# Kernel optimization log

Measured on AMD Instinct MI355X. Metric: run time of the kernel, lower is better.

## Reference

```python
import jax, jax.numpy as jnp
import numpy as np

GROUP_SIZE = 128  # quantization group size along K


def setup_inputs() -> dict:
    key = jax.random.key(0)
    k1, k2, k3, k4 = jax.random.split(key, 4)
    B, S, K = 2, 2048, 4096
    N = 11008
    num_groups = K // GROUP_SIZE
    x = jax.random.normal(k1, (B, S, K), dtype=jnp.float32)
    # int8 quantized weights, stored as int32 for portability (values in [-128, 127])
    qw = jax.random.randint(k2, (N, K), -128, 128, dtype=jnp.int32)
    # per-group scales (positive, small, like amax/127)
    sw = jax.random.uniform(k3, (N, num_groups), dtype=jnp.float32, minval=1e-4, maxval=0.02)
    bias = jax.random.normal(k4, (N,), dtype=jnp.float32)
    return {"x": x, "qw": qw, "sw": sw, "bias": bias}


def reference(x, qw, sw, bias):
    # x: [..., K], qw: [N, K] int8-valued, sw: [N, K//GROUP_SIZE], bias: [N]
    N, K = qw.shape
    num_groups = K // GROUP_SIZE
    # per-group dequantize: w[n, g, j] = qw[n, g, j] * sw[n, g]
    w_dequant = (qw.reshape(N, num_groups, GROUP_SIZE).astype(jnp.float32)
                 * sw[:, :, None]).reshape(N, K)
    x_dtype = x.dtype
    y = jnp.einsum('...k,nk->...n', x.astype(jnp.float32), w_dequant).astype(x_dtype)
    y = y + bias
    return y
```

## Files before the change

### kernel.cpp

```cpp
#include <hip/hip_runtime.h>


typedef __attribute__((ext_vector_type(8))) short short8;
typedef __attribute__((ext_vector_type(4))) float floatx4;

__device__ __forceinline__ unsigned short f2bf_rne(float f) {
  union { float f; unsigned int u; } c;
  c.f = f;
  unsigned int u = c.u;
  u += 0x7FFFu + ((u >> 16) & 1u);
  return (unsigned short)(u >> 16);
}

__global__ void prep_kernel(const float* __restrict__ x,
                            const int* __restrict__ qw,
                            const float* __restrict__ sw,
                            short* __restrict__ xb,
                            short* __restrict__ wb,
                            long nx_chunks, long total_chunks,
                            int K, int kshift, int gshift, int G, int ngroups) {
  long stride = (long)gridDim.x * blockDim.x;
  for (long c = (long)blockIdx.x * blockDim.x + threadIdx.x;
       c < total_chunks; c += stride) {
    if (c < nx_chunks) {
      long i = c * 8;
      const float4* p = (const float4*)(x + i);
      float4 a = p[0], b = p[1];
      short8 o;
      o[0] = (short)f2bf_rne(a.x); o[1] = (short)f2bf_rne(a.y);
      o[2] = (short)f2bf_rne(a.z); o[3] = (short)f2bf_rne(a.w);
      o[4] = (short)f2bf_rne(b.x); o[5] = (short)f2bf_rne(b.y);
      o[6] = (short)f2bf_rne(b.z); o[7] = (short)f2bf_rne(b.w);
      *(short8*)(xb + i) = o;
    } else {
      long e = (c - nx_chunks) * 8;
      int n, k;
      if (kshift >= 0) {
        n = (int)(e >> kshift);
        k = (int)(e & (long)(K - 1));
      } else {
        n = (int)(e / K);
        k = (int)(e - (long)n * K);
      }
      int g = (gshift >= 0) ? (k >> gshift) : (k / G);
      const int* q = qw + (long)n * K + k;
      float s = sw[(long)n * ngroups + g];
      int4 q0 = *(const int4*)q;
      int4 q1 = *(const int4*)(q + 4);
      short8 o;
      o[0] = (short)f2bf_rne((float)q0.x * s);
      o[1] = (short)f2bf_rne((float)q0.y * s);
      o[2] = (short)f2bf_rne((float)q0.z * s);
      o[3] = (short)f2bf_rne((float)q0.w * s);
      o[4] = (short)f2bf_rne((float)q1.x * s);
      o[5] = (short)f2bf_rne((float)q1.y * s);
      o[6] = (short)f2bf_rne((float)q1.z * s);
      o[7] = (short)f2bf_rne((float)q1.w * s);
      *(short8*)(wb + e) = o;
    }
  }
}

#define BM 256
#define BN 256
#define BK 64

__device__ __forceinline__ void stage_half(const short* __restrict__ src,
                                           int rowbase, int k0, int K,
                                           short* dst, int t) {
#pragma unroll
  for (int j = 0; j < 2; ++j) {
    const int c = (j << 9) | t;
    const int r = c >> 3;
    const int g = (c & 7) ^ (r & 7);
    __builtin_amdgcn_global_load_lds(
        (const __attribute__((address_space(1))) void*)(
            src + (long)(rowbase + r) * K + k0 + (g << 3)),
        (__attribute__((address_space(3))) void*)(dst + (c << 3)),
        16, 0, 0);
  }
}

__global__ __launch_bounds__(512, 2) void gemm8p_kernel(
    const short* __restrict__ Xb,
    const short* __restrict__ Wb,
    const float* __restrict__ bias,
    float* __restrict__ Y,
    int M, int N, int K) {
  __shared__ short As[2][2][128 * 64];
  __shared__ short Bs[2][2][128 * 64];

  const int t = threadIdx.x;
  const int wave = t >> 6;
  const int lane = t & 63;
  const int wm = wave >> 2;
  const int wn = wave & 3;
  const int quad = lane >> 4;
  const int l16 = lane & 15;

  const int gm = M / BM, gn = N / BN;
  int bid = (int)blockIdx.x;
  int mt, nt;
  if ((gm & 7) == 0) {
    int stripe = gm >> 3;
    int xcd = bid & 7;
    int q = bid >> 3;
    mt = xcd * stripe + q % stripe;
    nt = q / stripe;
  } else {
    mt = bid % gm;
    nt = bid / gm;
  }
  const long tileM = (long)mt * BM;
  const long tileN = (long)nt * BN;

  const short* __restrict__ Ag = Xb + tileM * K;
  const short* __restrict__ Bg = Wb + tileN * K;

  floatx4 acc[8][4];
#pragma unroll
  for (int i = 0; i < 8; ++i)
#pragma unroll
    for (int j = 0; j < 4; ++j) acc[i][j] = {0.f, 0.f, 0.f, 0.f};

  const int NT = K / BK;

  stage_half(Ag,   0,  0, K, &As[0][0][0], t);
  stage_half(Ag, 128,  0, K, &As[0][1][0], t);
  stage_half(Bg,   0,  0, K, &Bs[0][0][0], t);
  stage_half(Bg, 128,  0, K, &Bs[0][1][0], t);
  stage_half(Ag,   0, BK, K, &As[1][0][0], t);
  stage_half(Ag, 128, BK, K, &As[1][1][0], t);
  asm volatile("s_waitcnt vmcnt(4)" ::: "memory");
  __builtin_amdgcn_sched_barrier(0);
  __builtin_amdgcn_s_barrier();

  const int c0 = (quad ^ (l16 & 7)) << 3;
  const int c1 = c0 ^ 32;
  const int nb = (wn & 1) * 64;

  for (int T = 0; T < NT; ++T) {
    const int buf = T & 1;
    const short* Ab = &As[buf][wm][0];
    const short* Bb = &Bs[buf][wn >> 1][0];
    short8 a0[8], a1[8], b0[4], b1[4];

#pragma unroll
    for (int i = 0; i < 8; ++i)
      a0[i] = *(const short8*)(Ab + (i * 16 + l16) * 64 + c0);
#pragma unroll
    for (int j = 0; j < 4; ++j)
      b0[j] = *(const short8*)(Bb + (nb + j * 16 + l16) * 64 + c0);
    if (T + 1 < NT)
      stage_half(Bg, 0, (T + 1) * BK, K, &Bs[buf ^ 1][0][0], t);
    __builtin_amdgcn_sched_barrier(0);
    __builtin_amdgcn_s_barrier();
    asm volatile("s_waitcnt lgkmcnt(0)" ::: "memory");
    __builtin_amdgcn_sched_barrier(0);
    __builtin_amdgcn_s_setprio(1);
#pragma unroll
    for (int i = 0; i < 4; ++i)
#pragma unroll
      for (int j = 0; j < 4; ++j)
        acc[i][j] = __builtin_amdgcn_mfma_f32_16x16x32_bf16(a0[i], b0[j],
                                                            acc[i][j], 0, 0, 0);
    __builtin_amdgcn_s_setprio(0);
    __builtin_amdgcn_sched_barrier(0);
    __builtin_amdgcn_s_barrier();

#pragma unroll
    for (int i = 0; i < 8; ++i)
      a1[i] = *(const short8*)(Ab + (i * 16 + l16) * 64 + c1);
#pragma unroll
    for (int j = 0; j < 4; ++j)
      b1[j] = *(const short8*)(Bb + (nb + j * 16 + l16) * 64 + c1);
    if (T + 1 < NT)
      stage_half(Bg, 128, (T + 1) * BK, K, &Bs[buf ^ 1][1][0], t);
    __builtin_amdgcn_sched_barrier(0);
    __builtin_amdgcn_s_barrier();
    asm volatile("s_waitcnt lgkmcnt(0)" ::: "memory");
    __builtin_amdgcn_sched_barrier(0);
    __builtin_amdgcn_s_setprio(1);
#pragma unroll
    for (int i = 0; i < 4; ++i)
#pragma unroll
      for (int j = 0; j < 4; ++j)
        acc[4 + i][j] = __builtin_amdgcn_mfma_f32_16x16x32_bf16(
            a0[4 + i], b0[j], acc[4 + i][j], 0, 0, 0);
    __builtin_amdgcn_s_setprio(0);
    __builtin_amdgcn_sched_barrier(0);
    __builtin_amdgcn_s_barrier();

    if (T + 2 < NT)
      stage_half(Ag, 0, (T + 2) * BK, K, &As[buf][0][0], t);
    __builtin_amdgcn_sched_barrier(0);
    __builtin_amdgcn_s_barrier();
    asm volatile("s_waitcnt lgkmcnt(0)" ::: "memory");
    __builtin_amdgcn_sched_barrier(0);
    __builtin_amdgcn_s_setprio(1);
#pragma unroll
    for (int i = 0; i < 4; ++i)
#pragma unroll
      for (int j = 0; j < 4; ++j)
        acc[i][j] = __builtin_amdgcn_mfma_f32_16x16x32_bf16(a1[i], b1[j],
                                                            acc[i][j], 0, 0, 0);
    __builtin_amdgcn_s_setprio(0);
    __builtin_amdgcn_sched_barrier(0);
    __builtin_amdgcn_s_barrier();

    if (T + 2 < NT)
      stage_half(Ag, 128, (T + 2) * BK, K, &As[buf][1][0], t);
    __builtin_amdgcn_sched_barrier(0);
    __builtin_amdgcn_s_barrier();
    asm volatile("s_waitcnt lgkmcnt(0)" ::: "memory");
    __builtin_amdgcn_sched_barrier(0);
    __builtin_amdgcn_s_setprio(1);
#pragma unroll
    for (int i = 0; i < 4; ++i)
#pragma unroll
      for (int j = 0; j < 4; ++j)
        acc[4 + i][j] = __builtin_amdgcn_mfma_f32_16x16x32_bf16(
            a1[4 + i], b1[j], acc[4 + i][j], 0, 0, 0);
    __builtin_amdgcn_s_setprio(0);
    if (T + 2 < NT)
      asm volatile("s_waitcnt vmcnt(4)" ::: "memory");
    else
      asm volatile("s_waitcnt vmcnt(0)" ::: "memory");
    __builtin_amdgcn_sched_barrier(0);
    __builtin_amdgcn_s_barrier();
  }

  const long mbase = tileM + wm * 128;
  const long nbase = tileN + wn * 64;
#pragma unroll
  for (int j = 0; j < 4; ++j) {
    const long n = nbase + j * 16 + l16;
    const float bv = bias[n];
#pragma unroll
    for (int i = 0; i < 8; ++i) {
      const long m0 = mbase + i * 16 + quad * 4;
#pragma unroll
      for (int r = 0; r < 4; ++r)
        Y[(m0 + r) * (long)N + n] = acc[i][j][r] + bv;
    }
  }
}

__global__ void naive_kernel(const float* __restrict__ x,
                             const int* __restrict__ qw,
                             const float* __restrict__ sw,
                             const float* __restrict__ bias,
                             float* __restrict__ y,
                             int M, int N, int K, int G) {
  long idx = (long)blockIdx.x * blockDim.x + threadIdx.x;
  if (idx >= (long)M * N) return;
  int m = (int)(idx / N), n = (int)(idx % N);
  int ng = K / G;
  float acc = 0.f;
  for (int g = 0; g < ng; g++) {
    float s = sw[(long)n * ng + g];
    float part = 0.f;
    for (int k = g * G; k < (g + 1) * G; k++)
      part += x[(long)m * K + k] * (float)qw[(long)n * K + k];
    acc += part * s;
  }
  y[idx] = acc + bias[n];
}

extern "C" void kernel_launch(void* const* d_in, const int* in_sizes, int n_in,
                              void* d_out, int out_size, void* d_ws, size_t ws_size,
                              hipStream_t stream) {
  const float* x = (const float*)d_in[0];
  const int* qw = (const int*)d_in[1];
  const float* sw = (const float*)d_in[2];
  const float* bias = (const float*)d_in[3];
  float* y = (float*)d_out;

  const int N = in_sizes[3];
  const int K = in_sizes[1] / N;
  const int M = in_sizes[0] / K;
  const int ngroups = in_sizes[2] / N;
  const int G = K / ngroups;

  const long MK = (long)M * K;
  const long NK = (long)N * K;
  const size_t need = (size_t)(MK + NK) * sizeof(short);

  if (ws_size < need || (M % BM) || (N % BN) || (K % BK) || (K < 2 * BK) ||
      (G % 8)) {
    long total = (long)M * N;
    naive_kernel<<<(unsigned)((total + 255) / 256), 256, 0, stream>>>(
        x, qw, sw, bias, y, M, N, K, G);
    return;
  }

  short* xb = (short*)d_ws;
  short* wb = xb + MK;

  long nx_chunks = MK / 8;
  long total_chunks = nx_chunks + NK / 8;
  int kshift = ((K & (K - 1)) == 0) ? __builtin_ctz((unsigned)K) : -1;
  int gshift = ((G & (G - 1)) == 0) ? __builtin_ctz((unsigned)G) : -1;
  prep_kernel<<<2048, 256, 0, stream>>>(x, qw, sw, xb, wb,
                                        nx_chunks, total_chunks,
                                        K, kshift, gshift, G, ngroups);

  dim3 grid((unsigned)((M / BM) * (N / BN)));
  gemm8p_kernel<<<grid, 512, 0, stream>>>(xb, wb, bias, y, M, N, K);
}
```

Baseline: 736.2 us.

## Prefetch LDS fragments across iterations and split prep into separate x and w kernels

The GEMM main loop is rescheduled so the next tile's first A/B fragments are read from LDS at the end of the current iteration, and global-to-LDS staging is regrouped with different vmcnt waits. Most explicit lgkmcnt waits and sched_barriers are removed, so the compiler's own waits now enforce LDS read ordering and overlap between LDS reads and MFMAs. The single fused prep kernel becomes two kernels, one for x and one for the weights, which removes the per-element branch but adds a launch. Dropping the explicit waits risks hazards or worse scheduling if the compiler does not order the accesses as intended.

```diff
diff --git a/kernel.cpp b/kernel.cpp
--- a/kernel.cpp
+++ b/kernel.cpp
@@ -12,52 +12,53 @@
   return (unsigned short)(u >> 16);
 }
 
-__global__ void prep_kernel(const float* __restrict__ x,
-                            const int* __restrict__ qw,
-                            const float* __restrict__ sw,
-                            short* __restrict__ xb,
-                            short* __restrict__ wb,
-                            long nx_chunks, long total_chunks,
-                            int K, int kshift, int gshift, int G, int ngroups) {
+__global__ void prep_x_kernel(const float* __restrict__ x,
+                              short* __restrict__ xb, long nchunks) {
   long stride = (long)gridDim.x * blockDim.x;
   for (long c = (long)blockIdx.x * blockDim.x + threadIdx.x;
-       c < total_chunks; c += stride) {
-    if (c < nx_chunks) {
-      long i = c * 8;
-      const float4* p = (const float4*)(x + i);
-      float4 a = p[0], b = p[1];
-      short8 o;
-      o[0] = (short)f2bf_rne(a.x); o[1] = (short)f2bf_rne(a.y);
-      o[2] = (short)f2bf_rne(a.z); o[3] = (short)f2bf_rne(a.w);
-      o[4] = (short)f2bf_rne(b.x); o[5] = (short)f2bf_rne(b.y);
-      o[6] = (short)f2bf_rne(b.z); o[7] = (short)f2bf_rne(b.w);
-      *(short8*)(xb + i) = o;
+       c < nchunks; c += stride) {
+    const float4* p = (const float4*)(x + c * 8);
+    float4 a = p[0], b = p[1];
+    short8 o;
+    o[0] = (short)f2bf_rne(a.x); o[1] = (short)f2bf_rne(a.y);
+    o[2] = (short)f2bf_rne(a.z); o[3] = (short)f2bf_rne(a.w);
+    o[4] = (short)f2bf_rne(b.x); o[5] = (short)f2bf_rne(b.y);
+    o[6] = (short)f2bf_rne(b.z); o[7] = (short)f2bf_rne(b.w);
+    *(short8*)(xb + c * 8) = o;
+  }
+}
+
+__global__ void prep_w_kernel(const int* __restrict__ qw,
+                              const float* __restrict__ sw,
+                              short* __restrict__ wb, long nchunks,
+                              int kc, int kcshift, int gc, int gcshift,
+                              int ngroups) {
+  long stride = (long)gridDim.x * blockDim.x;
+  for (long c = (long)blockIdx.x * blockDim.x + threadIdx.x;
+       c < nchunks; c += stride) {
+    int n, kch;
+    if (kcshift >= 0) {
+      n = (int)(c >> kcshift);
+      kch = (int)(c & (long)(kc - 1));
     } else {
-      long e = (c - nx_chunks) * 8;
-      int n, k;
-      if (kshift >= 0) {
-        n = (int)(e >> kshift);
-        k = (int)(e & (long)(K - 1));
-      } else {
-        n = (int)(e / K);
-        k = (int)(e - (long)n * K);
-      }
-      int g = (gshift >= 0) ? (k >> gshift) : (k / G);
-      const int* q = qw + (long)n * K + k;
-      float s = sw[(long)n * ngroups + g];
-      int4 q0 = *(const int4*)q;
-      int4 q1 = *(const int4*)(q + 4);
-      short8 o;
-      o[0] = (short)f2bf_rne((float)q0.x * s);
-      o[1] = (short)f2bf_rne((float)q0.y * s);
-      o[2] = (short)f2bf_rne((float)q0.z * s);
-      o[3] = (short)f2bf_rne((float)q0.w * s);
-      o[4] = (short)f2bf_rne((float)q1.x * s);
-      o[5] = (short)f2bf_rne((float)q1.y * s);
-      o[6] = (short)f2bf_rne((float)q1.z * s);
-      o[7] = (short)f2bf_rne((float)q1.w * s);
-      *(short8*)(wb + e) = o;
+      n = (int)(c / kc);
+      kch = (int)(c - (long)n * kc);
     }
+    int g = (gcshift >= 0) ? (kch >> gcshift) : (kch / gc);
+    float s = sw[(long)n * ngroups + g];
+    const int* q = qw + c * 8;
+    int4 q0 = *(const int4*)q;
+    int4 q1 = *(const int4*)(q + 4);
+    short8 o;
+    o[0] = (short)f2bf_rne((float)q0.x * s);
+    o[1] = (short)f2bf_rne((float)q0.y * s);
+    o[2] = (short)f2bf_rne((float)q0.z * s);
+    o[3] = (short)f2bf_rne((float)q0.w * s);
+    o[4] = (short)f2bf_rne((float)q1.x * s);
+    o[5] = (short)f2bf_rne((float)q1.y * s);
+    o[6] = (short)f2bf_rne((float)q1.z * s);
+    o[7] = (short)f2bf_rne((float)q1.w * s);
+    *(short8*)(wb + c * 8) = o;
   }
 }
 
@@ -131,32 +132,44 @@
   stage_half(Bg, 128,  0, K, &Bs[0][1][0], t);
   stage_half(Ag,   0, BK, K, &As[1][0][0], t);
   stage_half(Ag, 128, BK, K, &As[1][1][0], t);
-  asm volatile("s_waitcnt vmcnt(4)" ::: "memory");
+  stage_half(Bg,   0, BK, K, &Bs[1][0][0], t);
+  asm volatile("s_waitcnt vmcnt(6)" ::: "memory");
+  __builtin_amdgcn_s_barrier();
+  asm volatile("" ::: "memory");
   __builtin_amdgcn_sched_barrier(0);
-  __builtin_amdgcn_s_barrier();
 
   const int c0 = (quad ^ (l16 & 7)) << 3;
   const int c1 = c0 ^ 32;
   const int nb = (wn & 1) * 64;
 
+  short8 a0[8], a1[8], b0[4], b1[4];
+  {
+    const short* Ab = &As[0][wm][0];
+    const short* Bb = &Bs[0][wn >> 1][0];
+#pragma unroll
+    for (int i = 0; i < 4; ++i)
+      a0[i] = *(const short8*)(Ab + (i * 16 + l16) * 64 + c0);
+#pragma unroll
+    for (int j = 0; j < 4; ++j)
+      b0[j] = *(const short8*)(Bb + (nb + j * 16 + l16) * 64 + c0);
+  }
+
   for (int T = 0; T < NT; ++T) {
     const int buf = T & 1;
-    const short* Ab = &As[buf][wm][0];
-    const short* Bb = &Bs[buf][wn >> 1][0];
-    short8 a0[8], a1[8], b0[4], b1[4];
-
+    const short* Ab  = &As[buf][wm][0];
+    const short* Bb  = &Bs[buf][wn >> 1][0];
+    const short* Abn = &As[buf ^ 1][wm][0];
+    const short* Bbn = &Bs[buf ^ 1][wn >> 1][0];
+
+    if (T + 1 < NT)
+      stage_half(Bg, 128, (T + 1) * BK, K, &Bs[buf ^ 1][1][0], t);
+#pragma unroll
+    for (int i = 0; i < 4; ++i)
+      a0[4 + i] = *(const short8*)(Ab + ((4 + i) * 16 + l16) * 64 + c0);
 #pragma unroll
     for (int i = 0; i < 8; ++i)
-      a0[i] = *(const short8*)(Ab + (i * 16 + l16) * 64 + c0);
-#pragma unroll
-    for (int j = 0; j < 4; ++j)
-      b0[j] = *(const short8*)(Bb + (nb + j * 16 + l16) * 64 + c0);
-    if (T + 1 < NT)
-      stage_half(Bg, 0, (T + 1) * BK, K, &Bs[buf ^ 1][0][0], t);
-    __builtin_amdgcn_sched_barrier(0);
-    __builtin_amdgcn_s_barrier();
-    asm volatile("s_waitcnt lgkmcnt(0)" ::: "memory");
-    __builtin_amdgcn_sched_barrier(0);
+      a1[i] = *(const short8*)(Ab + (i * 16 + l16) * 64 + c1);
+    __builtin_amdgcn_s_barrier();
     __builtin_amdgcn_s_setprio(1);
 #pragma unroll
     for (int i = 0; i < 4; ++i)
@@ -165,21 +178,12 @@
         acc[i][j] = __builtin_amdgcn_mfma_f32_16x16x32_bf16(a0[i], b0[j],
                                                             acc[i][j], 0, 0, 0);
     __builtin_amdgcn_s_setprio(0);
-    __builtin_amdgcn_sched_barrier(0);
-    __builtin_amdgcn_s_barrier();
-
-#pragma unroll
-    for (int i = 0; i < 8; ++i)
-      a1[i] = *(const short8*)(Ab + (i * 16 + l16) * 64 + c1);
+    __builtin_amdgcn_s_barrier();
+
 #pragma unroll
     for (int j = 0; j < 4; ++j)
       b1[j] = *(const short8*)(Bb + (nb + j * 16 + l16) * 64 + c1);
-    if (T + 1 < NT)
-      stage_half(Bg, 128, (T + 1) * BK, K, &Bs[buf ^ 1][1][0], t);
-    __builtin_amdgcn_sched_barrier(0);
-    __builtin_amdgcn_s_barrier();
-    asm volatile("s_waitcnt lgkmcnt(0)" ::: "memory");
-    __builtin_amdgcn_sched_barrier(0);
+    __builtin_amdgcn_s_barrier();
     __builtin_amdgcn_s_setprio(1);
 #pragma unroll
     for (int i = 0; i < 4; ++i)
@@ -188,15 +192,11 @@
         acc[4 + i][j] = __builtin_amdgcn_mfma_f32_16x16x32_bf16(
             a0[4 + i], b0[j], acc[4 + i][j], 0, 0, 0);
     __builtin_amdgcn_s_setprio(0);
-    __builtin_amdgcn_sched_barrier(0);
     __builtin_amdgcn_s_barrier();
 
     if (T + 2 < NT)
       stage_half(Ag, 0, (T + 2) * BK, K, &As[buf][0][0], t);
-    __builtin_amdgcn_sched_barrier(0);
-    __builtin_amdgcn_s_barrier();
-    asm volatile("s_waitcnt lgkmcnt(0)" ::: "memory");
-    __builtin_amdgcn_sched_barrier(0);
+    __builtin_amdgcn_s_barrier();
     __builtin_amdgcn_s_setprio(1);
 #pragma unroll
     for (int i = 0; i < 4; ++i)
@@ -205,15 +205,26 @@
         acc[i][j] = __builtin_amdgcn_mfma_f32_16x16x32_bf16(a1[i], b1[j],
                                                             acc[i][j], 0, 0, 0);
     __builtin_amdgcn_s_setprio(0);
+    __builtin_amdgcn_s_barrier();
+
+    if (T + 2 < NT) {
+      stage_half(Ag, 128, (T + 2) * BK, K, &As[buf][1][0], t);
+      stage_half(Bg, 0, (T + 2) * BK, K, &Bs[buf][0][0], t);
+      asm volatile("s_waitcnt vmcnt(6)" ::: "memory");
+    } else {
+      asm volatile("s_waitcnt vmcnt(0)" ::: "memory");
+    }
+    __builtin_amdgcn_s_barrier();
+    asm volatile("" ::: "memory");
     __builtin_amdgcn_sched_barrier(0);
-    __builtin_amdgcn_s_barrier();
-
-    if (T + 2 < NT)
-      stage_half(Ag, 128, (T + 2) * BK, K, &As[buf][1][0], t);
-    __builtin_amdgcn_sched_barrier(0);
-    __builtin_amdgcn_s_barrier();
-    asm volatile("s_waitcnt lgkmcnt(0)" ::: "memory");
-    __builtin_amdgcn_sched_barrier(0);
+    if (T + 1 < NT) {
+#pragma unroll
+      for (int i = 0; i < 4; ++i)
+        a0[i] = *(const short8*)(Abn + (i * 16 + l16) * 64 + c0);
+#pragma unroll
+      for (int j = 0; j < 4; ++j)
+        b0[j] = *(const short8*)(Bbn + (nb + j * 16 + l16) * 64 + c0);
+    }
     __builtin_amdgcn_s_setprio(1);
 #pragma unroll
     for (int i = 0; i < 4; ++i)
@@ -222,11 +233,6 @@
         acc[4 + i][j] = __builtin_amdgcn_mfma_f32_16x16x32_bf16(
             a1[4 + i], b1[j], acc[4 + i][j], 0, 0, 0);
     __builtin_amdgcn_s_setprio(0);
-    if (T + 2 < NT)
-      asm volatile("s_waitcnt vmcnt(4)" ::: "memory");
-    else
-      asm volatile("s_waitcnt vmcnt(0)" ::: "memory");
-    __builtin_amdgcn_sched_barrier(0);
     __builtin_amdgcn_s_barrier();
   }
 
@@ -297,13 +303,14 @@
   short* xb = (short*)d_ws;
   short* wb = xb + MK;
 
-  long nx_chunks = MK / 8;
-  long total_chunks = nx_chunks + NK / 8;
-  int kshift = ((K & (K - 1)) == 0) ? __builtin_ctz((unsigned)K) : -1;
-  int gshift = ((G & (G - 1)) == 0) ? __builtin_ctz((unsigned)G) : -1;
-  prep_kernel<<<2048, 256, 0, stream>>>(x, qw, sw, xb, wb,
-                                        nx_chunks, total_chunks,
-                                        K, kshift, gshift, G, ngroups);
+  const int kc = K / 8;
+  const int gc = G / 8;
+  int kcshift = ((kc & (kc - 1)) == 0) ? __builtin_ctz((unsigned)kc) : -1;
+  int gcshift = ((gc & (gc - 1)) == 0) ? __builtin_ctz((unsigned)gc) : -1;
+
+  prep_x_kernel<<<2048, 256, 0, stream>>>(x, xb, MK / 8);
+  prep_w_kernel<<<2048, 256, 0, stream>>>(qw, sw, wb, NK / 8,
+                                          kc, kcshift, gc, gcshift, ngroups);
 
   dim3 grid((unsigned)((M / BM) * (N / BN)));
   gemm8p_kernel<<<grid, 512, 0, stream>>>(xb, wb, bias, y, M, N, K);
```

Measured after the change: 873.4 us. +18.6%, slower.
